# Kernel optimization log

Hardware: AMD Instinct MI355X
Metric: run time of the kernel (lower is better)

The kernel has to match this reference:

```python
import jax, jax.numpy as jnp
import numpy as np
from jax import lax

T, D, H = 8192, 2048, 256  # seq_len, feature dim, lstm hidden (= D/8)


def _lstm(x, W, U, b, reverse=False):
    """Keras LSTM with activation='sigmoid', recurrent_activation='sigmoid'.
    x: (T, Din); W: (Din, 4H); U: (H, 4H); b: (4H,). Gate order i,f,c,o."""
    if reverse:
        x = x[::-1]
    zx = x @ W + b  # precompute input projection for all timesteps: (T, 4H)
    h0 = jnp.zeros((U.shape[0],), x.dtype)

    def step(carry, z):
        h, c = carry
        z = z + h @ U
        i, f, g, o = jnp.split(z, 4)
        c = jax.nn.sigmoid(f) * c + jax.nn.sigmoid(i) * jax.nn.sigmoid(g)
        h = jax.nn.sigmoid(o) * jax.nn.sigmoid(c)
        return (h, c), h

    _, hs = lax.scan(step, (h0, h0), zx)
    return hs[::-1] if reverse else hs


def _bilstm(x, Wf, Uf, bf, Wb, Ub, bb):
    # Bidirectional merge_mode='concat'
    return jnp.concatenate(
        [_lstm(x, Wf, Uf, bf), _lstm(x, Wb, Ub, bb, reverse=True)], axis=-1)


def setup_inputs() -> dict:
    key = jax.random.key(0)
    ks = jax.random.split(key, 13)
    s = 0.02
    f32 = jnp.float32
    return {
        "x": jax.random.normal(ks[0], (T, D), f32),
        "W1f": s * jax.random.normal(ks[1], (D, 4 * H), f32),
        "U1f": s * jax.random.normal(ks[2], (H, 4 * H), f32),
        "b1f": jnp.zeros((4 * H,), f32),
        "W1b": s * jax.random.normal(ks[3], (D, 4 * H), f32),
        "U1b": s * jax.random.normal(ks[4], (H, 4 * H), f32),
        "b1b": jnp.zeros((4 * H,), f32),
        "W2f": s * jax.random.normal(ks[5], (2 * H, 4 * H), f32),
        "U2f": s * jax.random.normal(ks[6], (H, 4 * H), f32),
        "b2f": jnp.zeros((4 * H,), f32),
        "W2b": s * jax.random.normal(ks[7], (2 * H, 4 * H), f32),
        "U2b": s * jax.random.normal(ks[8], (H, 4 * H), f32),
        "b2b": jnp.zeros((4 * H,), f32),
    }


def reference(x, W1f, U1f, b1f, W1b, U1b, b1b,
              W2f, U2f, b2f, W2b, U2b, b2b):
    M1 = _bilstm(x, W1f, U1f, b1f, W1b, U1b, b1b)    # (T, 2H) = (T, D/4)
    M2 = _bilstm(M1, W2f, U2f, b2f, W2b, U2b, b2b)   # (T, D/4)
    temp1 = jnp.concatenate([x, M1], axis=1)          # (T, 5D/4)
    temp2 = jnp.concatenate([x, M2], axis=1)          # (T, 5D/4)
    return jnp.stack([temp1, temp2], axis=0)          # (2, T, 5D/4)
```

## Files before the change

kernel.cpp:

```cpp
#include <hip/hip_runtime.h>
#include <stdint.h>

#define T_STEPS 8192
#define DIN     2048
#define NH      256
#define G4      1024
#define OUTW    2560

__device__ __forceinline__ float sigf(float x) {
    return 1.0f / (1.0f + __expf(-x));
}

__device__ __forceinline__ int dot4(int a, int b, int c) {
#if __has_builtin(__builtin_amdgcn_sdot4)
    return __builtin_amdgcn_sdot4(a, b, c, false);
#else
    int r = c;
#pragma unroll
    for (int i = 0; i < 4; ++i) {
        int ai = (a << (24 - 8 * i)) >> 24;
        int bi = (b << (24 - 8 * i)) >> 24;
        r += ai * bi;
    }
    return r;
#endif
}

__global__ void quant_u_kernel(const float* __restrict__ U0, const float* __restrict__ U1,
                               const float* __restrict__ U2, const float* __restrict__ U3,
                               uint32_t* __restrict__ uq, float* __restrict__ sc) {
    const float* U = (blockIdx.x == 0) ? U0 : (blockIdx.x == 1) ? U1
                   : (blockIdx.x == 2) ? U2 : U3;
    uint32_t* uqo = uq + (size_t)blockIdx.x * (NH / 4) * G4;
    float* sco = sc + (size_t)blockIdx.x * G4;

    int j = threadIdx.x;
    float ma = 0.f;
    for (int k = 0; k < NH; ++k) ma = fmaxf(ma, fabsf(U[(size_t)k * G4 + j]));
    float inv = (ma > 0.f) ? 127.f / ma : 0.f;
    sco[j] = ma * (1.0f / (127.f * 127.f));
    for (int w = 0; w < NH / 4; ++w) {
        uint32_t word = 0;
#pragma unroll
        for (int b = 0; b < 4; ++b) {
            float v = U[(size_t)(4 * w + b) * G4 + j];
            int q = __float2int_rn(v * inv);
            q = max(-127, min(127, q));
            word |= ((uint32_t)(q & 0xff)) << (8 * b);
        }
        uqo[(size_t)w * G4 + j] = word;
    }
}

__global__ void copy_x_kernel(const float4* __restrict__ x4, float* __restrict__ out) {
    const int total = 2 * T_STEPS * (DIN / 4);
    for (int i = blockIdx.x * blockDim.x + threadIdx.x; i < total;
         i += gridDim.x * blockDim.x) {
        int o   = i >> 22;
        int rem = i & ((1 << 22) - 1);
        int t   = rem >> 9;
        int c4  = rem & 511;
        float4 v = x4[(size_t)t * 512 + c4];
        *(float4*)(out + (size_t)o * T_STEPS * OUTW + (size_t)t * OUTW + (size_t)c4 * 4) = v;
    }
}

__global__ __launch_bounds__(256) void gemm_zx_kernel(
    const float* __restrict__ A, int lda,
    const float* __restrict__ B, const float* __restrict__ bias,
    float* __restrict__ C, int K) {
    __shared__ float As[64][17];
    __shared__ float Bs[16][68];
    int tid = threadIdx.x;
    int bm = blockIdx.y * 64, bn = blockIdx.x * 64;
    int trow = tid >> 4, tcol = tid & 15;
    int ar = tid >> 2, ac = (tid & 3) * 4;
    int br = tid >> 4, bc = (tid & 15) * 4;
    float acc[4][4] = {};

    for (int k0 = 0; k0 < K; k0 += 16) {
        float4 av = *(const float4*)(A + (size_t)(bm + ar) * lda + k0 + ac);
        float4 bv = *(const float4*)(B + (size_t)(k0 + br) * G4 + bn + bc);
        As[ar][ac + 0] = av.x; As[ar][ac + 1] = av.y;
        As[ar][ac + 2] = av.z; As[ar][ac + 3] = av.w;
        Bs[br][bc + 0] = bv.x; Bs[br][bc + 1] = bv.y;
        Bs[br][bc + 2] = bv.z; Bs[br][bc + 3] = bv.w;
        __syncthreads();
#pragma unroll
        for (int kk = 0; kk < 16; ++kk) {
            float af[4], bf[4];
#pragma unroll
            for (int i = 0; i < 4; ++i) af[i] = As[trow * 4 + i][kk];
#pragma unroll
            for (int i = 0; i < 4; ++i) bf[i] = Bs[kk][tcol * 4 + i];
#pragma unroll
            for (int i = 0; i < 4; ++i)
#pragma unroll
                for (int j = 0; j < 4; ++j)
                    acc[i][j] = fmaf(af[i], bf[j], acc[i][j]);
        }
        __syncthreads();
    }
#pragma unroll
    for (int i = 0; i < 4; ++i) {
        float4 v;
        v.x = acc[i][0] + bias[bn + tcol * 4 + 0];
        v.y = acc[i][1] + bias[bn + tcol * 4 + 1];
        v.z = acc[i][2] + bias[bn + tcol * 4 + 2];
        v.w = acc[i][3] + bias[bn + tcol * 4 + 3];
        *(float4*)(C + (size_t)(bm + trow * 4 + i) * G4 + bn + tcol * 4) = v;
    }
}

__global__ __launch_bounds__(1024, 4) void lstm_scan_kernel(
    const float* __restrict__ Zxf, const float* __restrict__ Zxb,
    const uint32_t* __restrict__ Uqf, const uint32_t* __restrict__ Uqb,
    const float* __restrict__ scf, const float* __restrict__ scb,
    float* __restrict__ outbase) {
    __shared__ float z_lds[G4];
    __shared__ int4 hq_lds4[16];

    const int dir = blockIdx.x;
    const float* Zx = dir ? Zxb : Zxf;
    const uint32_t* Uq = dir ? Uqb : Uqf;
    const float* sc = dir ? scb : scf;

    const int j = threadIdx.x;

    int u[64];
#pragma unroll
    for (int w = 0; w < 64; ++w) u[w] = (int)Uq[(size_t)w * G4 + j];
#pragma unroll
    for (int w = 0; w < 64; w += 4)
        asm volatile("" : "+v"(u[w]), "+v"(u[w + 1]), "+v"(u[w + 2]), "+v"(u[w + 3]));

    const float scj = sc[j];

    if (j < 16) hq_lds4[j] = make_int4(0, 0, 0, 0);
    float c = 0.f;

    const int step = dir ? -1 : 1;
    int t = dir ? (T_STEPS - 1) : 0;
    float zx = Zx[(size_t)t * G4 + j];
    float* outp = outbase + 2048 + dir * NH;
    __syncthreads();

    for (int s = 0; s < T_STEPS; ++s) {
        const int tn = (s + 1 < T_STEPS) ? t + step : t;
        const float nzx = Zx[(size_t)tn * G4 + j];

        int acc = 0;
#pragma unroll
        for (int w4 = 0; w4 < 16; ++w4) {
            const int4 hw = hq_lds4[w4];
            acc = dot4(u[4 * w4 + 0], hw.x, acc);
            acc = dot4(u[4 * w4 + 1], hw.y, acc);
            acc = dot4(u[4 * w4 + 2], hw.z, acc);
            acc = dot4(u[4 * w4 + 3], hw.w, acc);
        }
        z_lds[j] = zx + (float)acc * scj;
        __syncthreads();

        if (j < NH) {
            float zi = z_lds[j];
            float zf = z_lds[j + NH];
            float zg = z_lds[j + 2 * NH];
            float zo = z_lds[j + 3 * NH];
            c = sigf(zf) * c + sigf(zi) * sigf(zg);
            float h = sigf(zo) * sigf(c);
            outp[(size_t)t * OUTW + j] = h;
            int q = __float2int_rn(h * 127.f);
            q = max(0, min(127, q));
            ((uint8_t*)hq_lds4)[j] = (uint8_t)q;
        }
        __syncthreads();

        zx = nzx;
        t = tn;
    }
}

extern "C" void kernel_launch(void* const* d_in, const int* in_sizes, int n_in,
                              void* d_out, int out_size, void* d_ws, size_t ws_size,
                              hipStream_t stream) {
    const float* x   = (const float*)d_in[0];
    const float* W1f = (const float*)d_in[1];
    const float* U1f = (const float*)d_in[2];
    const float* b1f = (const float*)d_in[3];
    const float* W1b = (const float*)d_in[4];
    const float* U1b = (const float*)d_in[5];
    const float* b1b = (const float*)d_in[6];
    const float* W2f = (const float*)d_in[7];
    const float* U2f = (const float*)d_in[8];
    const float* b2f = (const float*)d_in[9];
    const float* W2b = (const float*)d_in[10];
    const float* U2b = (const float*)d_in[11];
    const float* b2b = (const float*)d_in[12];

    float* out  = (float*)d_out;
    float* out1 = out + (size_t)T_STEPS * OUTW;

    float* Zxf = (float*)d_ws;
    float* Zxb = Zxf + (size_t)T_STEPS * G4;
    uint32_t* uq = (uint32_t*)(Zxb + (size_t)T_STEPS * G4);
    float* scq = (float*)(uq + (size_t)4 * 64 * G4);

    quant_u_kernel<<<4, 1024, 0, stream>>>(U1f, U1b, U2f, U2b, uq, scq);

    copy_x_kernel<<<2048, 256, 0, stream>>>((const float4*)x, out);

    dim3 gg(16, 128);
    gemm_zx_kernel<<<gg, 256, 0, stream>>>(x, DIN, W1f, b1f, Zxf, DIN);
    gemm_zx_kernel<<<gg, 256, 0, stream>>>(x, DIN, W1b, b1b, Zxb, DIN);

    lstm_scan_kernel<<<2, 1024, 0, stream>>>(Zxf, Zxb,
                                             uq + (size_t)0 * 64 * G4, uq + (size_t)1 * 64 * G4,
                                             scq + 0 * G4, scq + 1 * G4, out);

    gemm_zx_kernel<<<gg, 256, 0, stream>>>(out + 2048, OUTW, W2f, b2f, Zxf, 512);
    gemm_zx_kernel<<<gg, 256, 0, stream>>>(out + 2048, OUTW, W2b, b2b, Zxb, 512);

    lstm_scan_kernel<<<2, 1024, 0, stream>>>(Zxf, Zxb,
                                             uq + (size_t)2 * 64 * G4, uq + (size_t)3 * 64 * G4,
                                             scq + 2 * G4, scq + 3 * G4, out1);
}
```

Before: 16.99 ms.

## Apply gate sigmoids in parallel phase and prefetch input projection two steps ahead

All 1024 threads now apply the sigmoid to their own gate pre-activation before the barrier. The serial 256-thread phase then needs only one sigmoid (on c) instead of five, which shortens the critical path of each recurrent step. The Zx load is prefetched two timesteps ahead instead of one to hide global memory latency better. The launch bounds are replaced with explicit AMDGPU attributes pinning waves per EU to 4.

```diff
diff --git a/kernel.cpp b/kernel.cpp
--- a/kernel.cpp
+++ b/kernel.cpp
@@ -112,12 +112,13 @@
     }
 }
 
-__global__ __launch_bounds__(1024, 4) void lstm_scan_kernel(
+__global__ __attribute__((amdgpu_flat_work_group_size(1024, 1024)))
+__attribute__((amdgpu_waves_per_eu(4, 4))) void lstm_scan_kernel(
     const float* __restrict__ Zxf, const float* __restrict__ Zxb,
     const uint32_t* __restrict__ Uqf, const uint32_t* __restrict__ Uqb,
     const float* __restrict__ scf, const float* __restrict__ scb,
     float* __restrict__ outbase) {
-    __shared__ float z_lds[G4];
+    __shared__ float s_lds[G4];
     __shared__ int4 hq_lds4[16];
 
     const int dir = blockIdx.x;
@@ -140,14 +141,17 @@
     float c = 0.f;
 
     const int step = dir ? -1 : 1;
-    int t = dir ? (T_STEPS - 1) : 0;
-    float zx = Zx[(size_t)t * G4 + j];
+    const int t0 = dir ? (T_STEPS - 1) : 0;
+    float zx0 = Zx[(size_t)t0 * G4 + j];
+    float zx1 = Zx[(size_t)(t0 + step) * G4 + j];
     float* outp = outbase + 2048 + dir * NH;
     __syncthreads();
 
+    int t = t0;
     for (int s = 0; s < T_STEPS; ++s) {
-        const int tn = (s + 1 < T_STEPS) ? t + step : t;
-        const float nzx = Zx[(size_t)tn * G4 + j];
+        int t2 = t + 2 * step;
+        t2 = (t2 < 0) ? 0 : (t2 >= T_STEPS ? T_STEPS - 1 : t2);
+        const float zx2 = Zx[(size_t)t2 * G4 + j];
 
         int acc = 0;
 #pragma unroll
@@ -158,16 +162,16 @@
             acc = dot4(u[4 * w4 + 2], hw.z, acc);
             acc = dot4(u[4 * w4 + 3], hw.w, acc);
         }
-        z_lds[j] = zx + (float)acc * scj;
+        s_lds[j] = sigf(zx0 + (float)acc * scj);
         __syncthreads();
 
         if (j < NH) {
-            float zi = z_lds[j];
-            float zf = z_lds[j + NH];
-            float zg = z_lds[j + 2 * NH];
-            float zo = z_lds[j + 3 * NH];
-            c = sigf(zf) * c + sigf(zi) * sigf(zg);
-            float h = sigf(zo) * sigf(c);
+            float si = s_lds[j];
+            float sf = s_lds[j + NH];
+            float sg = s_lds[j + 2 * NH];
+            float so = s_lds[j + 3 * NH];
+            c = sf * c + si * sg;
+            float h = so * sigf(c);
             outp[(size_t)t * OUTW + j] = h;
             int q = __float2int_rn(h * 127.f);
             q = max(0, min(127, q));
@@ -175,8 +179,8 @@
         }
         __syncthreads();
 
-        zx = nzx;
-        t = tn;
+        zx0 = zx1; zx1 = zx2;
+        t += step;
     }
 }
 
@@ -206,7 +210,6 @@
     float* scq = (float*)(uq + (size_t)4 * 64 * G4);
 
     quant_u_kernel<<<4, 1024, 0, stream>>>(U1f, U1b, U2f, U2b, uq, scq);
-
     copy_x_kernel<<<2048, 256, 0, stream>>>((const float4*)x, out);
 
     dim3 gg(16, 128);
```

New measurement: 18.24 ms. +7.3%, slower.
